# Optimization experiments

Hardware: AMD Instinct MI355X
Metric: run time of the kernel (lower is better)

## Reference

```python
import jax, jax.numpy as jnp
import numpy as np
from jax import lax

TAGSET_SIZE = 50
K = TAGSET_SIZE + 2          # +START, +STOP
START_TAG = TAGSET_SIZE      # 50
STOP_TAG = TAGSET_SIZE + 1   # 51
B, T = 1024, 512
NEG_INF = -10000.0


def setup_inputs() -> dict:
    key = jax.random.key(0)
    k1, k2, k3, k4 = jax.random.split(key, 4)
    logits = jax.random.normal(k1, (B, T, K), dtype=jnp.float32)
    transitions = jax.random.normal(k2, (K, K), dtype=jnp.float32)
    labels = jax.random.randint(k3, (B, T), 0, TAGSET_SIZE)          # real tags only
    lens = jax.random.randint(k4, (B,), 1, T + 1)                    # at least 1 token
    return {"logits": logits, "transitions": transitions, "labels": labels, "lens": lens}


def _crf_nll(logits, transitions, labels, lens):
    b, t, k = logits.shape

    # ---- forward algorithm (log partition) ----
    alpha0 = jnp.full((b, k), NEG_INF, dtype=logits.dtype).at[:, START_TAG].set(0.0)
    step_mask = jnp.arange(t)[None, :] < lens[:, None]               # [B,T] True while c_lens > 0

    def step(alpha, inp):
        logit_t, m_t = inp                                           # [B,K], [B]
        # alpha_nxt[b,i] = logsumexp_j(trans[i,j] + alpha[b,j]) + logit[b,i]
        mat = alpha[:, None, :] + transitions[None, :, :]            # [B,K,K]
        alpha_nxt = jax.nn.logsumexp(mat, axis=2) + logit_t
        alpha = jnp.where(m_t[:, None], alpha_nxt, alpha)
        return alpha, None

    alpha, _ = lax.scan(step, alpha0, (jnp.swapaxes(logits, 0, 1), step_mask.T))
    alpha = alpha + transitions[STOP_TAG][None, :]
    partition = jax.nn.logsumexp(alpha, axis=1)                      # [B]

    # ---- transition score of gold path ----
    start_col = jnp.full((b, 1), START_TAG, dtype=labels.dtype)
    stop_col = jnp.full((b, 1), STOP_TAG, dtype=labels.dtype)
    labels_ext = jnp.concatenate([start_col, labels, stop_col], axis=1)  # [B,T+2]
    pos = jnp.arange(t + 2)[None, :]
    keep = pos < (lens + 1)[:, None]                                 # positions <= lens keep tag, rest -> STOP
    labels_ext = jnp.where(keep, labels_ext, STOP_TAG)
    prev, nxt = labels_ext[:, :-1], labels_ext[:, 1:]                # [B,T+1]
    trn_scr = transitions[nxt, prev]                                 # trans[next, prev]
    m_trn = (jnp.arange(t + 1)[None, :] < (lens + 1)[:, None]).astype(logits.dtype)
    transition_score = jnp.sum(trn_scr * m_trn, axis=1)              # [B]

    # ---- emission score of gold path ----
    em = jnp.take_along_axis(logits, labels[:, :, None], axis=2)[:, :, 0]  # [B,T]
    m_em = (jnp.arange(t)[None, :] < lens[:, None]).astype(logits.dtype)
    emission_score = jnp.sum(em * m_em, axis=1)                      # [B]

    # faithful to source: partition + emission - transition
    return partition + emission_score - transition_score


def reference(logits, transitions, labels, lens):
    return _crf_nll(logits, transitions, labels, lens)
```

## Files before the change

kernel.cpp:

```cpp
#include <hip/hip_runtime.h>
#include <hip/hip_bf16.h>

#define KTAG 52
#define START_TAG 50
#define STOP_TAG 51
#define TMAX 512

__device__ __forceinline__ float rdlane(float v, int l) {
    return __int_as_float(__builtin_amdgcn_readlane(__float_as_int(v), l));
}

__global__ __launch_bounds__(64) void crf_nll_kernel(
    const float* __restrict__ logits,
    const float* __restrict__ trans,
    const int*   __restrict__ labels,
    const int*   __restrict__ lens,
    float* __restrict__ out)
{
    constexpr float L2E = 1.4426950408889634f;
    constexpr float LN2 = 0.6931471805599453f;

    const int b    = blockIdx.x;
    const int lane = threadIdx.x;
    const bool active = lane < KTAG;
    const int len = lens[b];

    float Erow[KTAG];
    {
        const float* trow = trans + (size_t)(active ? lane : 0) * KTAG;
        #pragma unroll
        for (int j = 0; j < KTAG; ++j)
            Erow[j] = active ? exp2f(trow[j] * L2E) : 0.0f;
    }

    const float* lgp = logits + (size_t)b * TMAX * KTAG + (active ? lane : 0);

    float beta = (lane == START_TAG) ? 1.0f : 0.0f;
    float M2 = 0.0f;

    auto lgt = [&](int t) -> float {
        int tc = t < TMAX ? t : (TMAX - 1);
        return lgp[tc * KTAG];
    };

    auto STEP = [&](float lg, float scl) {
        float e = exp2f(lg * L2E) * scl;
        float a0 = 0.f, a1 = 0.f, a2 = 0.f, a3 = 0.f;
        #pragma unroll
        for (int j = 0; j < 13; ++j) {
            a0 = fmaf(Erow[4*j+0], rdlane(beta, 4*j+0), a0);
            a1 = fmaf(Erow[4*j+1], rdlane(beta, 4*j+1), a1);
            a2 = fmaf(Erow[4*j+2], rdlane(beta, 4*j+2), a2);
            a3 = fmaf(Erow[4*j+3], rdlane(beta, 4*j+3), a3);
        }
        beta = ((a0 + a1) + (a2 + a3)) * e;
    };

    float l0 = lgt(0), l1 = lgt(1), l2 = lgt(2), l3 = lgt(3);

    int t = 0;
    while (t + 4 <= len) {
        float n0 = lgt(t + 4), n1 = lgt(t + 5), n2 = lgt(t + 6), n3 = lgt(t + 7);
        float scl = 1.0f;
        if (t > 0) {
            float m = rdlane(beta, 0);
            M2 += log2f(m);
            scl = 1.0f / m;
        }
        STEP(l0, scl);
        STEP(l1, 1.0f);
        STEP(l2, 1.0f);
        STEP(l3, 1.0f);
        l0 = n0; l1 = n1; l2 = n2; l3 = n3;
        t += 4;
    }
    if (t < len) {
        float scl = 1.0f;
        if (t > 0) {
            float m = rdlane(beta, 0);
            M2 += log2f(m);
            scl = 1.0f / m;
        }
        STEP(l0, scl); ++t;
        if (t < len) { STEP(l1, 1.0f); ++t; }
        if (t < len) { STEP(l2, 1.0f); ++t; }
    }

    float es = active ? trans[(size_t)STOP_TAG * KTAG + lane] : 0.0f;
    float contrib = active ? beta * exp2f(es * L2E) : 0.0f;
    float s = contrib;
    #pragma unroll
    for (int off = 32; off; off >>= 1) s += __shfl_xor(s, off);
    float partition = LN2 * (M2 + log2f(s));

    const int*   labp = labels + (size_t)b * TMAX;
    const float* lgb  = logits + (size_t)b * TMAX * KTAG;
    float em = 0.0f, tr = 0.0f;
    for (int tt = lane; tt < len; tt += 64) {
        int lab = labp[tt];
        em += lgb[tt * KTAG + lab];
        int prv = (tt == 0) ? START_TAG : labp[tt - 1];
        tr += trans[lab * KTAG + prv];
    }
    if (lane == 0)
        tr += trans[STOP_TAG * KTAG + labp[len - 1]];

    #pragma unroll
    for (int off = 32; off; off >>= 1) {
        em += __shfl_xor(em, off);
        tr += __shfl_xor(tr, off);
    }

    if (lane == 0) out[b] = partition + em - tr;
}

extern "C" void kernel_launch(void* const* d_in, const int* in_sizes, int n_in,
                              void* d_out, int out_size, void* d_ws, size_t ws_size,
                              hipStream_t stream) {
    const float* logits = (const float*)d_in[0];
    const float* trans  = (const float*)d_in[1];
    const int*   labels = (const int*)d_in[2];
    const int*   lens   = (const int*)d_in[3];
    float* out = (float*)d_out;

    const int B = in_sizes[3];
    crf_nll_kernel<<<dim3(B), dim3(64), 0, stream>>>(logits, trans, labels, lens, out);
}
```

Before: 116.7 us.

## Sort sequences by length and pair short with long per wavefront

Adds a rank kernel that builds a length-sorted permutation of the batch. Each wavefront then processes two sequences, the i-th shortest and the i-th longest, interleaving the two recurrences to balance work and hide latency. The matrix-vector step now reads beta from shared memory with packed FMA instead of 52 readlane broadcasts. This costs an extra kernel launch and workspace use, and adds an LDS write/read dependency on every step.

```diff
diff --git a/kernel.cpp b/kernel.cpp
--- a/kernel.cpp
+++ b/kernel.cpp
@@ -6,112 +6,169 @@
 #define STOP_TAG 51
 #define TMAX 512
 
+typedef float v2f __attribute__((ext_vector_type(2)));
+
 __device__ __forceinline__ float rdlane(float v, int l) {
     return __int_as_float(__builtin_amdgcn_readlane(__float_as_int(v), l));
 }
 
-__global__ __launch_bounds__(64) void crf_nll_kernel(
+__device__ __forceinline__ void pk_fma(v2f& acc, v2f a, v2f b) {
+    asm("v_pk_fma_f32 %0, %1, %2, %0" : "+v"(acc) : "v"(a), "v"(b));
+}
+
+#define LPL 16
+__global__ __launch_bounds__(64) void rank_kernel(
+    const int* __restrict__ lens, int* __restrict__ perm, int B)
+{
+    const int lane = threadIdx.x;
+    int myl[LPL];
+    #pragma unroll
+    for (int k = 0; k < LPL; ++k) {
+        int j = lane * LPL + k;
+        myl[k] = (j < B) ? lens[j] : 0x7fffffff;
+    }
+    const int base = blockIdx.x * 64;
+    for (int i = 0; i < 64; ++i) {
+        int b = base + i;
+        if (b >= B) break;
+        int Lb = lens[b];
+        int r = 0;
+        #pragma unroll
+        for (int k = 0; k < LPL; ++k) {
+            int j = lane * LPL + k;
+            r += (myl[k] < Lb || (myl[k] == Lb && j < b)) ? 1 : 0;
+        }
+        #pragma unroll
+        for (int off = 32; off; off >>= 1) r += __shfl_xor(r, off);
+        if (lane == 0) perm[r] = b;
+    }
+}
+
+__global__ __launch_bounds__(64) void crf_pair_kernel(
     const float* __restrict__ logits,
     const float* __restrict__ trans,
     const int*   __restrict__ labels,
     const int*   __restrict__ lens,
-    float* __restrict__ out)
+    const int*   __restrict__ perm,
+    float* __restrict__ out, int B)
 {
     constexpr float L2E = 1.4426950408889634f;
     constexpr float LN2 = 0.6931471805599453f;
 
-    const int b    = blockIdx.x;
+    const int w    = blockIdx.x;
     const int lane = threadIdx.x;
     const bool active = lane < KTAG;
-    const int len = lens[b];
 
-    float Erow[KTAG];
+    const int iA = w, iB = B - 1 - w;
+    const bool hasB = (iB != iA);
+    const int bA = perm[iA];
+    const int bB = hasB ? perm[iB] : bA;
+    const int nA = lens[bA];
+    const int nB = lens[bB];
+
+    __shared__ __align__(16) float sA[64], sB[64];
+
+    v2f Epk[26];
+    float stopE;
     {
         const float* trow = trans + (size_t)(active ? lane : 0) * KTAG;
         #pragma unroll
-        for (int j = 0; j < KTAG; ++j)
-            Erow[j] = active ? exp2f(trow[j] * L2E) : 0.0f;
+        for (int p = 0; p < 13; ++p) {
+            float4 q = *reinterpret_cast<const float4*>(&trow[4 * p]);
+            v2f lo, hi;
+            lo.x = active ? exp2f(q.x * L2E) : 0.f;
+            lo.y = active ? exp2f(q.y * L2E) : 0.f;
+            hi.x = active ? exp2f(q.z * L2E) : 0.f;
+            hi.y = active ? exp2f(q.w * L2E) : 0.f;
+            Epk[2 * p] = lo; Epk[2 * p + 1] = hi;
+        }
+        stopE = active ? exp2f(trans[(size_t)STOP_TAG * KTAG + lane] * L2E) : 0.f;
     }
 
-    const float* lgp = logits + (size_t)b * TMAX * KTAG + (active ? lane : 0);
+    const float* lgA = logits + (size_t)bA * TMAX * KTAG + (active ? lane : 0);
+    const float* lgB = logits + (size_t)bB * TMAX * KTAG + (active ? lane : 0);
 
-    float beta = (lane == START_TAG) ? 1.0f : 0.0f;
-    float M2 = 0.0f;
+    float betaA = (lane == START_TAG) ? 1.f : 0.f;
+    float betaB = betaA;
+    sA[lane] = betaA;
+    sB[lane] = betaB;
+    float M2A = 0.f, M2B = 0.f;
 
-    auto lgt = [&](int t) -> float {
-        int tc = t < TMAX ? t : (TMAX - 1);
-        return lgp[tc * KTAG];
+    auto ldA = [&](int t) { int tc = t < TMAX ? t : (TMAX - 1); return lgA[tc * KTAG]; };
+    auto ldB = [&](int t) { int tc = t < TMAX ? t : (TMAX - 1); return lgB[tc * KTAG]; };
+
+    float a0 = ldA(0), a1 = ldA(1), a2 = ldA(2), a3 = ldA(3);
+    float b0 = ldB(0), b1 = ldB(1), b2 = ldB(2), b3 = ldB(3);
+
+    auto MATV = [&](float* s, float e) -> float {
+        v2f ac0 = {0.f, 0.f}, ac1 = {0.f, 0.f};
+        #pragma unroll
+        for (int p = 0; p < 13; ++p) {
+            float4 q = *reinterpret_cast<const float4*>(&s[4 * p]);
+            v2f lo; lo.x = q.x; lo.y = q.y;
+            v2f hi; hi.x = q.z; hi.y = q.w;
+            pk_fma(ac0, Epk[2 * p], lo);
+            pk_fma(ac1, Epk[2 * p + 1], hi);
+        }
+        return ((ac0.x + ac0.y) + (ac1.x + ac1.y)) * e;
     };
 
-    auto STEP = [&](float lg, float scl) {
-        float e = exp2f(lg * L2E) * scl;
-        float a0 = 0.f, a1 = 0.f, a2 = 0.f, a3 = 0.f;
+    int t = 0;
+    for (; t < nA; ++t) {
+        float sclA = 1.f, sclB = 1.f;
+        if (((t & 3) == 0) && t) {
+            float mA = rdlane(betaA, 0), mB = rdlane(betaB, 0);
+            M2A += log2f(mA); M2B += log2f(mB);
+            sclA = 1.f / mA;  sclB = 1.f / mB;
+        }
+        float eA = exp2f(a0 * L2E) * sclA;
+        a0 = a1; a1 = a2; a2 = a3; a3 = ldA(t + 4);
+        betaA = MATV(sA, eA);
+        sA[lane] = betaA;
+        float eB = exp2f(b0 * L2E) * sclB;
+        b0 = b1; b1 = b2; b2 = b3; b3 = ldB(t + 4);
+        betaB = MATV(sB, eB);
+        sB[lane] = betaB;
+    }
+    for (; t < nB; ++t) {
+        float sclB = 1.f;
+        if (((t & 3) == 0) && t) {
+            float mB = rdlane(betaB, 0);
+            M2B += log2f(mB);
+            sclB = 1.f / mB;
+        }
+        float eB = exp2f(b0 * L2E) * sclB;
+        b0 = b1; b1 = b2; b2 = b3; b3 = ldB(t + 4);
+        betaB = MATV(sB, eB);
+        sB[lane] = betaB;
+    }
+
+    auto FINISH = [&](float beta, float M2, int b, int len) {
+        float s = beta * stopE;
         #pragma unroll
-        for (int j = 0; j < 13; ++j) {
-            a0 = fmaf(Erow[4*j+0], rdlane(beta, 4*j+0), a0);
-            a1 = fmaf(Erow[4*j+1], rdlane(beta, 4*j+1), a1);
-            a2 = fmaf(Erow[4*j+2], rdlane(beta, 4*j+2), a2);
-            a3 = fmaf(Erow[4*j+3], rdlane(beta, 4*j+3), a3);
+        for (int off = 32; off; off >>= 1) s += __shfl_xor(s, off);
+        float partition = LN2 * (M2 + log2f(s));
+
+        const int*   labp = labels + (size_t)b * TMAX;
+        const float* lgb  = logits + (size_t)b * TMAX * KTAG;
+        float em = 0.f, tr = 0.f;
+        for (int tt = lane; tt < len; tt += 64) {
+            int lab = labp[tt];
+            em += lgb[tt * KTAG + lab];
+            int prv = (tt == 0) ? START_TAG : labp[tt - 1];
+            tr += trans[lab * KTAG + prv];
         }
-        beta = ((a0 + a1) + (a2 + a3)) * e;
+        if (lane == 0) tr += trans[STOP_TAG * KTAG + labp[len - 1]];
+        #pragma unroll
+        for (int off = 32; off; off >>= 1) {
+            em += __shfl_xor(em, off);
+            tr += __shfl_xor(tr, off);
+        }
+        if (lane == 0) out[b] = partition + em - tr;
     };
 
-    float l0 = lgt(0), l1 = lgt(1), l2 = lgt(2), l3 = lgt(3);
-
-    int t = 0;
-    while (t + 4 <= len) {
-        float n0 = lgt(t + 4), n1 = lgt(t + 5), n2 = lgt(t + 6), n3 = lgt(t + 7);
-        float scl = 1.0f;
-        if (t > 0) {
-            float m = rdlane(beta, 0);
-            M2 += log2f(m);
-            scl = 1.0f / m;
-        }
-        STEP(l0, scl);
-        STEP(l1, 1.0f);
-        STEP(l2, 1.0f);
-        STEP(l3, 1.0f);
-        l0 = n0; l1 = n1; l2 = n2; l3 = n3;
-        t += 4;
-    }
-    if (t < len) {
-        float scl = 1.0f;
-        if (t > 0) {
-            float m = rdlane(beta, 0);
-            M2 += log2f(m);
-            scl = 1.0f / m;
-        }
-        STEP(l0, scl); ++t;
-        if (t < len) { STEP(l1, 1.0f); ++t; }
-        if (t < len) { STEP(l2, 1.0f); ++t; }
-    }
-
-    float es = active ? trans[(size_t)STOP_TAG * KTAG + lane] : 0.0f;
-    float contrib = active ? beta * exp2f(es * L2E) : 0.0f;
-    float s = contrib;
-    #pragma unroll
-    for (int off = 32; off; off >>= 1) s += __shfl_xor(s, off);
-    float partition = LN2 * (M2 + log2f(s));
-
-    const int*   labp = labels + (size_t)b * TMAX;
-    const float* lgb  = logits + (size_t)b * TMAX * KTAG;
-    float em = 0.0f, tr = 0.0f;
-    for (int tt = lane; tt < len; tt += 64) {
-        int lab = labp[tt];
-        em += lgb[tt * KTAG + lab];
-        int prv = (tt == 0) ? START_TAG : labp[tt - 1];
-        tr += trans[lab * KTAG + prv];
-    }
-    if (lane == 0)
-        tr += trans[STOP_TAG * KTAG + labp[len - 1]];
-
-    #pragma unroll
-    for (int off = 32; off; off >>= 1) {
-        em += __shfl_xor(em, off);
-        tr += __shfl_xor(tr, off);
-    }
-
-    if (lane == 0) out[b] = partition + em - tr;
+    FINISH(betaA, M2A, bA, nA);
+    if (hasB) FINISH(betaB, M2B, bB, nB);
 }
 
 extern "C" void kernel_launch(void* const* d_in, const int* in_sizes, int n_in,
@@ -124,5 +181,9 @@
     float* out = (float*)d_out;
 
     const int B = in_sizes[3];
-    crf_nll_kernel<<<dim3(B), dim3(64), 0, stream>>>(logits, trans, labels, lens, out);
+    int* perm = (int*)d_ws;
+
+    rank_kernel<<<dim3((B + 63) / 64), dim3(64), 0, stream>>>(lens, perm, B);
+    crf_pair_kernel<<<dim3((B + 1) / 2), dim3(64), 0, stream>>>(
+        logits, trans, labels, lens, perm, out, B);
 }
```

New measurement: 209.8 us. +79.8%, slower.

## Split CRF forward recursion into forward/backward halves and sort batches by length

Applied to the files above, without the earlier changes.

Each sequence is now processed by two waves: one runs the forward recursion over the first half of the timesteps, the other runs a backward recursion over the second half, and the two are combined with a dot product to form the partition. This halves the serial dependency chain per sequence. A separate rank kernel computes a length-sorted permutation so that blocks are interleaved across CUs for load balance. The cost is an extra kernel launch, a workspace buffer, and a shared-memory sync, and the backward wave also does the gold-path scoring.

```diff
diff --git a/kernel.cpp b/kernel.cpp
--- a/kernel.cpp
+++ b/kernel.cpp
@@ -5,113 +5,174 @@
 #define START_TAG 50
 #define STOP_TAG 51
 #define TMAX 512
+#define NCU 256
 
 __device__ __forceinline__ float rdlane(float v, int l) {
     return __int_as_float(__builtin_amdgcn_readlane(__float_as_int(v), l));
 }
 
-__global__ __launch_bounds__(64) void crf_nll_kernel(
+__device__ __forceinline__ float matv(const float* __restrict__ Erow, float v) {
+    float a0 = 0.f, a1 = 0.f, a2 = 0.f, a3 = 0.f;
+    #pragma unroll
+    for (int j = 0; j < 13; ++j) {
+        a0 = fmaf(Erow[4*j+0], rdlane(v, 4*j+0), a0);
+        a1 = fmaf(Erow[4*j+1], rdlane(v, 4*j+1), a1);
+        a2 = fmaf(Erow[4*j+2], rdlane(v, 4*j+2), a2);
+        a3 = fmaf(Erow[4*j+3], rdlane(v, 4*j+3), a3);
+    }
+    return (a0 + a1) + (a2 + a3);
+}
+
+template<bool BWD>
+__device__ __forceinline__ float chain(const float* __restrict__ p0, int stride,
+                                       int maxk, int nsteps, const float* __restrict__ Erow,
+                                       float beta, float& M2) {
+    constexpr float L2E = 1.4426950408889634f;
+    M2 = 0.f;
+
+    auto lgt = [&](int k) -> float {
+        int kc = k < maxk ? k : maxk;
+        return p0[(long)stride * kc];
+    };
+    auto STEP = [&](float lg, float scl) {
+        float e = exp2f(lg * L2E) * scl;
+        if (BWD) beta = matv(Erow, beta * e);
+        else     beta = matv(Erow, beta) * e;
+    };
+
+    float l0 = lgt(0), l1 = lgt(1), l2 = lgt(2), l3 = lgt(3);
+    int k = 0;
+    while (k + 4 <= nsteps) {
+        float n0 = lgt(k+4), n1 = lgt(k+5), n2 = lgt(k+6), n3 = lgt(k+7);
+        float scl = 1.f;
+        if (k > 0) {
+            float m = rdlane(beta, 0);
+            M2 += log2f(m);
+            scl = 1.f / m;
+        }
+        STEP(l0, scl); STEP(l1, 1.f); STEP(l2, 1.f); STEP(l3, 1.f);
+        l0 = n0; l1 = n1; l2 = n2; l3 = n3;
+        k += 4;
+    }
+    if (k < nsteps) {
+        float scl = 1.f;
+        if (k > 0) {
+            float m = rdlane(beta, 0);
+            M2 += log2f(m);
+            scl = 1.f / m;
+        }
+        STEP(l0, scl); ++k;
+        if (k < nsteps) { STEP(l1, 1.f); ++k; }
+        if (k < nsteps) { STEP(l2, 1.f); ++k; }
+    }
+    return beta;
+}
+
+#define LPL 16
+__global__ __launch_bounds__(64) void rank_kernel(
+    const int* __restrict__ lens, int* __restrict__ perm, int B)
+{
+    const int lane = threadIdx.x;
+    int myl[LPL];
+    #pragma unroll
+    for (int k = 0; k < LPL; ++k) {
+        int j = lane * LPL + k;
+        myl[k] = (j < B) ? lens[j] : 0x7fffffff;
+    }
+    const int base = blockIdx.x * 64;
+    for (int i = 0; i < 64; ++i) {
+        int b = base + i;
+        if (b >= B) break;
+        int Lb = lens[b];
+        int r = 0;
+        #pragma unroll
+        for (int k = 0; k < LPL; ++k) {
+            int j = lane * LPL + k;
+            r += (myl[k] < Lb || (myl[k] == Lb && j < b)) ? 1 : 0;
+        }
+        #pragma unroll
+        for (int off = 32; off; off >>= 1) r += __shfl_xor(r, off);
+        if (lane == 0) perm[r] = b;
+    }
+}
+
+__global__ __launch_bounds__(128) void crf_split_kernel(
     const float* __restrict__ logits,
     const float* __restrict__ trans,
     const int*   __restrict__ labels,
     const int*   __restrict__ lens,
-    float* __restrict__ out)
+    const int*   __restrict__ perm,
+    float* __restrict__ out, int B)
 {
     constexpr float L2E = 1.4426950408889634f;
     constexpr float LN2 = 0.6931471805599453f;
 
-    const int b    = blockIdx.x;
-    const int lane = threadIdx.x;
+    const int blk  = blockIdx.x;
+    const int wave = threadIdx.x >> 6;
+    const int lane = threadIdx.x & 63;
     const bool active = lane < KTAG;
-    const int len = lens[b];
+    const bool bwd = (wave == 1);
+
+    int r = blk;
+    if ((B % NCU) == 0) {
+        int per = B / NCU;
+        r = (blk % NCU) * per + (blk / NCU);
+    }
+    const int batch = perm[r];
+    const int len = lens[batch];
+    const int mid = len >> 1;
 
     float Erow[KTAG];
-    {
-        const float* trow = trans + (size_t)(active ? lane : 0) * KTAG;
-        #pragma unroll
-        for (int j = 0; j < KTAG; ++j)
-            Erow[j] = active ? exp2f(trow[j] * L2E) : 0.0f;
+    #pragma unroll
+    for (int j = 0; j < KTAG; ++j) {
+        float tv = active ? (bwd ? trans[j * KTAG + lane]
+                                 : trans[(size_t)lane * KTAG + j]) : 0.f;
+        Erow[j] = active ? exp2f(tv * L2E) : 0.f;
     }
 
-    const float* lgp = logits + (size_t)b * TMAX * KTAG + (active ? lane : 0);
+    const float* base = logits + (size_t)batch * TMAX * KTAG + (active ? lane : 0);
 
-    float beta = (lane == START_TAG) ? 1.0f : 0.0f;
-    float M2 = 0.0f;
-
-    auto lgt = [&](int t) -> float {
-        int tc = t < TMAX ? t : (TMAX - 1);
-        return lgp[tc * KTAG];
-    };
-
-    auto STEP = [&](float lg, float scl) {
-        float e = exp2f(lg * L2E) * scl;
-        float a0 = 0.f, a1 = 0.f, a2 = 0.f, a3 = 0.f;
-        #pragma unroll
-        for (int j = 0; j < 13; ++j) {
-            a0 = fmaf(Erow[4*j+0], rdlane(beta, 4*j+0), a0);
-            a1 = fmaf(Erow[4*j+1], rdlane(beta, 4*j+1), a1);
-            a2 = fmaf(Erow[4*j+2], rdlane(beta, 4*j+2), a2);
-            a3 = fmaf(Erow[4*j+3], rdlane(beta, 4*j+3), a3);
-        }
-        beta = ((a0 + a1) + (a2 + a3)) * e;
-    };
-
-    float l0 = lgt(0), l1 = lgt(1), l2 = lgt(2), l3 = lgt(3);
-
-    int t = 0;
-    while (t + 4 <= len) {
-        float n0 = lgt(t + 4), n1 = lgt(t + 5), n2 = lgt(t + 6), n3 = lgt(t + 7);
-        float scl = 1.0f;
-        if (t > 0) {
-            float m = rdlane(beta, 0);
-            M2 += log2f(m);
-            scl = 1.0f / m;
-        }
-        STEP(l0, scl);
-        STEP(l1, 1.0f);
-        STEP(l2, 1.0f);
-        STEP(l3, 1.0f);
-        l0 = n0; l1 = n1; l2 = n2; l3 = n3;
-        t += 4;
-    }
-    if (t < len) {
-        float scl = 1.0f;
-        if (t > 0) {
-            float m = rdlane(beta, 0);
-            M2 += log2f(m);
-            scl = 1.0f / m;
-        }
-        STEP(l0, scl); ++t;
-        if (t < len) { STEP(l1, 1.0f); ++t; }
-        if (t < len) { STEP(l2, 1.0f); ++t; }
+    float M2, beta;
+    if (bwd) {
+        float b0 = active ? exp2f(trans[STOP_TAG * KTAG + lane] * L2E) : 0.f;
+        beta = chain<true>(base + (size_t)(len - 1) * KTAG, -KTAG,
+                           len - 1, len - mid, Erow, b0, M2);
+    } else {
+        float b0 = (lane == START_TAG) ? 1.f : 0.f;
+        beta = chain<false>(base, KTAG, TMAX - 1, mid, Erow, b0, M2);
     }
 
-    float es = active ? trans[(size_t)STOP_TAG * KTAG + lane] : 0.0f;
-    float contrib = active ? beta * exp2f(es * L2E) : 0.0f;
-    float s = contrib;
-    #pragma unroll
-    for (int off = 32; off; off >>= 1) s += __shfl_xor(s, off);
-    float partition = LN2 * (M2 + log2f(s));
+    __shared__ float sB[64];
+    __shared__ float sM2f;
+    if (!bwd) {
+        sB[lane] = beta;
+        if (lane == 0) sM2f = M2;
+    }
+    __syncthreads();
 
-    const int*   labp = labels + (size_t)b * TMAX;
-    const float* lgb  = logits + (size_t)b * TMAX * KTAG;
-    float em = 0.0f, tr = 0.0f;
-    for (int tt = lane; tt < len; tt += 64) {
-        int lab = labp[tt];
-        em += lgb[tt * KTAG + lab];
-        int prv = (tt == 0) ? START_TAG : labp[tt - 1];
-        tr += trans[lab * KTAG + prv];
+    if (bwd) {
+        float d = beta * sB[lane];
+        #pragma unroll
+        for (int off = 32; off; off >>= 1) d += __shfl_xor(d, off);
+        float partition = LN2 * (sM2f + M2 + log2f(d));
+
+        const int*   labp = labels + (size_t)batch * TMAX;
+        const float* lgb  = logits + (size_t)batch * TMAX * KTAG;
+        float em = 0.f, tr = 0.f;
+        for (int tt = lane; tt < len; tt += 64) {
+            int lab = labp[tt];
+            em += lgb[tt * KTAG + lab];
+            int prv = (tt == 0) ? START_TAG : labp[tt - 1];
+            tr += trans[lab * KTAG + prv];
+        }
+        if (lane == 0) tr += trans[STOP_TAG * KTAG + labp[len - 1]];
+        #pragma unroll
+        for (int off = 32; off; off >>= 1) {
+            em += __shfl_xor(em, off);
+            tr += __shfl_xor(tr, off);
+        }
+        if (lane == 0) out[batch] = partition + em - tr;
     }
-    if (lane == 0)
-        tr += trans[STOP_TAG * KTAG + labp[len - 1]];
-
-    #pragma unroll
-    for (int off = 32; off; off >>= 1) {
-        em += __shfl_xor(em, off);
-        tr += __shfl_xor(tr, off);
-    }
-
-    if (lane == 0) out[b] = partition + em - tr;
 }
 
 extern "C" void kernel_launch(void* const* d_in, const int* in_sizes, int n_in,
@@ -124,5 +185,9 @@
     float* out = (float*)d_out;
 
     const int B = in_sizes[3];
-    crf_nll_kernel<<<dim3(B), dim3(64), 0, stream>>>(logits, trans, labels, lens, out);
+    int* perm = (int*)d_ws;
+
+    rank_kernel<<<dim3((B + 63) / 64), dim3(64), 0, stream>>>(lens, perm, B);
+    crf_split_kernel<<<dim3(B), dim3(128), 0, stream>>>(
+        logits, trans, labels, lens, perm, out, B);
 }
```

Measured after the change: 152.2 us. 30.5% more time.

## Run forward and backward CRF recursions concurrently meeting at sequence midpoint

Applied to the files above, without the earlier changes.

Splits the serial forward-algorithm recursion into a forward pass over the first half and a backward pass over the second half, interleaved in the same wavefront. The partition is recovered by a dot product of the two messages at the midpoint. This roughly halves the length of the serial dependency chain per batch row, at the cost of twice the registers for transition matrices (forward and transposed copies) and more readlane traffic per step. The gold-path score loop is also unrolled with all loads issued before the reduction.

```diff
diff --git a/kernel.cpp b/kernel.cpp
--- a/kernel.cpp
+++ b/kernel.cpp
@@ -1,16 +1,15 @@
 #include <hip/hip_runtime.h>
-#include <hip/hip_bf16.h>
 
 #define KTAG 52
 #define START_TAG 50
 #define STOP_TAG 51
 #define TMAX 512
 
-__device__ __forceinline__ float rdlane(float v, int l) {
+__device__ __forceinline__ float rdlanef(float v, int l) {
     return __int_as_float(__builtin_amdgcn_readlane(__float_as_int(v), l));
 }
 
-__global__ __launch_bounds__(64) void crf_nll_kernel(
+__global__ __launch_bounds__(64, 1) void crf_fused_kernel(
     const float* __restrict__ logits,
     const float* __restrict__ trans,
     const int*   __restrict__ labels,
@@ -24,87 +23,133 @@
     const int lane = threadIdx.x;
     const bool active = lane < KTAG;
     const int len = lens[b];
+    const int mid = len >> 1;
 
-    float Erow[KTAG];
-    {
-        const float* trow = trans + (size_t)(active ? lane : 0) * KTAG;
-        #pragma unroll
-        for (int j = 0; j < KTAG; ++j)
-            Erow[j] = active ? exp2f(trow[j] * L2E) : 0.0f;
+    float EF[KTAG], EB[KTAG];
+    #pragma unroll
+    for (int j = 0; j < KTAG; ++j) {
+        float tf = active ? trans[(size_t)lane * KTAG + j] : 0.f;
+        float tb = active ? trans[(size_t)j * KTAG + lane] : 0.f;
+        EF[j] = active ? exp2f(tf * L2E) : 0.f;
+        EB[j] = active ? exp2f(tb * L2E) : 0.f;
     }
 
-    const float* lgp = logits + (size_t)b * TMAX * KTAG + (active ? lane : 0);
+    const float* pF = logits + (size_t)b * TMAX * KTAG + (active ? lane : 0);
+    const float* pB = pF + (size_t)(len - 1) * KTAG;
 
-    float beta = (lane == START_TAG) ? 1.0f : 0.0f;
-    float M2 = 0.0f;
-
-    auto lgt = [&](int t) -> float {
-        int tc = t < TMAX ? t : (TMAX - 1);
-        return lgp[tc * KTAG];
+    auto lgF = [&](int k) -> float {
+        int kc = k < TMAX - 1 ? k : TMAX - 1;
+        return pF[(long)KTAG * kc];
+    };
+    auto lgB = [&](int k) -> float {
+        int kc = k < len - 1 ? k : len - 1;
+        return pB[-(long)KTAG * kc];
     };
 
-    auto STEP = [&](float lg, float scl) {
-        float e = exp2f(lg * L2E) * scl;
+    float betaF = (lane == START_TAG) ? 1.f : 0.f;
+    float gamma = active ? exp2f(trans[STOP_TAG * KTAG + lane] * L2E) : 0.f;
+    float M2F = 0.f, M2B = 0.f;
+
+    auto STEP2 = [&](float lf, float sf, float lb, float sb) {
+        float eF = exp2f(lf * L2E);
+        float eB = exp2f(lb * L2E);
+        float xF = betaF * sf;
+        float xB = gamma * sb * eB;
+        float fa0 = 0.f, fa1 = 0.f, fa2 = 0.f, fa3 = 0.f;
+        float ba0 = 0.f, ba1 = 0.f, ba2 = 0.f, ba3 = 0.f;
+        #pragma unroll
+        for (int p = 0; p < 13; ++p) {
+            fa0 = fmaf(EF[4*p+0], rdlanef(xF, 4*p+0), fa0);
+            ba0 = fmaf(EB[4*p+0], rdlanef(xB, 4*p+0), ba0);
+            fa1 = fmaf(EF[4*p+1], rdlanef(xF, 4*p+1), fa1);
+            ba1 = fmaf(EB[4*p+1], rdlanef(xB, 4*p+1), ba1);
+            fa2 = fmaf(EF[4*p+2], rdlanef(xF, 4*p+2), fa2);
+            ba2 = fmaf(EB[4*p+2], rdlanef(xB, 4*p+2), ba2);
+            fa3 = fmaf(EF[4*p+3], rdlanef(xF, 4*p+3), fa3);
+            ba3 = fmaf(EB[4*p+3], rdlanef(xB, 4*p+3), ba3);
+        }
+        betaF = ((fa0 + fa1) + (fa2 + fa3)) * eF;
+        gamma = ((ba0 + ba1) + (ba2 + ba3));
+    };
+    auto STEPB = [&](float lb, float sb) {
+        float eB = exp2f(lb * L2E);
+        float xB = gamma * sb * eB;
         float a0 = 0.f, a1 = 0.f, a2 = 0.f, a3 = 0.f;
         #pragma unroll
-        for (int j = 0; j < 13; ++j) {
-            a0 = fmaf(Erow[4*j+0], rdlane(beta, 4*j+0), a0);
-            a1 = fmaf(Erow[4*j+1], rdlane(beta, 4*j+1), a1);
-            a2 = fmaf(Erow[4*j+2], rdlane(beta, 4*j+2), a2);
-            a3 = fmaf(Erow[4*j+3], rdlane(beta, 4*j+3), a3);
+        for (int p = 0; p < 13; ++p) {
+            a0 = fmaf(EB[4*p+0], rdlanef(xB, 4*p+0), a0);
+            a1 = fmaf(EB[4*p+1], rdlanef(xB, 4*p+1), a1);
+            a2 = fmaf(EB[4*p+2], rdlanef(xB, 4*p+2), a2);
+            a3 = fmaf(EB[4*p+3], rdlanef(xB, 4*p+3), a3);
         }
-        beta = ((a0 + a1) + (a2 + a3)) * e;
+        gamma = (a0 + a1) + (a2 + a3);
     };
 
-    float l0 = lgt(0), l1 = lgt(1), l2 = lgt(2), l3 = lgt(3);
+    float f0 = lgF(0), f1 = lgF(1), f2 = lgF(2), f3 = lgF(3);
+    float g0 = lgB(0), g1 = lgB(1), g2 = lgB(2), g3 = lgB(3);
 
     int t = 0;
-    while (t + 4 <= len) {
-        float n0 = lgt(t + 4), n1 = lgt(t + 5), n2 = lgt(t + 6), n3 = lgt(t + 7);
-        float scl = 1.0f;
+    while (t + 4 <= mid) {
+        float nf0 = lgF(t+4), nf1 = lgF(t+5), nf2 = lgF(t+6), nf3 = lgF(t+7);
+        float ng0 = lgB(t+4), ng1 = lgB(t+5), ng2 = lgB(t+6), ng3 = lgB(t+7);
+        float sF = 1.f, sB = 1.f;
         if (t > 0) {
-            float m = rdlane(beta, 0);
-            M2 += log2f(m);
-            scl = 1.0f / m;
+            float mF = fmaxf(rdlanef(betaF, 0), 1e-30f);
+            float mB = fmaxf(rdlanef(gamma, 0), 1e-30f);
+            M2F += log2f(mF); sF = 1.f / mF;
+            M2B += log2f(mB); sB = 1.f / mB;
         }
-        STEP(l0, scl);
-        STEP(l1, 1.0f);
-        STEP(l2, 1.0f);
-        STEP(l3, 1.0f);
-        l0 = n0; l1 = n1; l2 = n2; l3 = n3;
+        STEP2(f0, sF, g0, sB);
+        STEP2(f1, 1.f, g1, 1.f);
+        STEP2(f2, 1.f, g2, 1.f);
+        STEP2(f3, 1.f, g3, 1.f);
+        f0 = nf0; f1 = nf1; f2 = nf2; f3 = nf3;
+        g0 = ng0; g1 = ng1; g2 = ng2; g3 = ng3;
         t += 4;
     }
-    if (t < len) {
-        float scl = 1.0f;
+    const int r = mid - t;
+    if (r > 0) {
+        float sF = 1.f, sB = 1.f;
         if (t > 0) {
-            float m = rdlane(beta, 0);
-            M2 += log2f(m);
-            scl = 1.0f / m;
+            float mF = fmaxf(rdlanef(betaF, 0), 1e-30f);
+            float mB = fmaxf(rdlanef(gamma, 0), 1e-30f);
+            M2F += log2f(mF); sF = 1.f / mF;
+            M2B += log2f(mB); sB = 1.f / mB;
         }
-        STEP(l0, scl); ++t;
-        if (t < len) { STEP(l1, 1.0f); ++t; }
-        if (t < len) { STEP(l2, 1.0f); ++t; }
+        STEP2(f0, sF, g0, sB);
+        if (r > 1) STEP2(f1, 1.f, g1, 1.f);
+        if (r > 2) STEP2(f2, 1.f, g2, 1.f);
+    }
+    if (len - mid > mid) {
+        float gl = (r == 0) ? g0 : (r == 1) ? g1 : (r == 2) ? g2 : g3;
+        STEPB(gl, 1.f);
     }
 
-    float es = active ? trans[(size_t)STOP_TAG * KTAG + lane] : 0.0f;
-    float contrib = active ? beta * exp2f(es * L2E) : 0.0f;
-    float s = contrib;
+    float d = gamma * betaF;
     #pragma unroll
-    for (int off = 32; off; off >>= 1) s += __shfl_xor(s, off);
-    float partition = LN2 * (M2 + log2f(s));
+    for (int off = 32; off; off >>= 1) d += __shfl_xor(d, off);
+    float partition = LN2 * (M2F + M2B + log2f(d));
 
     const int*   labp = labels + (size_t)b * TMAX;
     const float* lgb  = logits + (size_t)b * TMAX * KTAG;
-    float em = 0.0f, tr = 0.0f;
-    for (int tt = lane; tt < len; tt += 64) {
-        int lab = labp[tt];
-        em += lgb[tt * KTAG + lab];
-        int prv = (tt == 0) ? START_TAG : labp[tt - 1];
-        tr += trans[lab * KTAG + prv];
+    int lab[8], prv[8]; bool msk[8];
+    #pragma unroll
+    for (int c = 0; c < 8; ++c) {
+        int tt = c * 64 + lane;
+        msk[c] = tt < len;
+        int ttc = msk[c] ? tt : 0;
+        lab[c] = labp[ttc];
+        prv[c] = (ttc == 0) ? START_TAG : labp[ttc - 1];
     }
-    if (lane == 0)
-        tr += trans[STOP_TAG * KTAG + labp[len - 1]];
-
+    float em = 0.f, tr = 0.f;
+    #pragma unroll
+    for (int c = 0; c < 8; ++c) {
+        int ttc = msk[c] ? (c * 64 + lane) : 0;
+        float ev = lgb[(size_t)ttc * KTAG + lab[c]];
+        float tv = trans[lab[c] * KTAG + prv[c]];
+        if (msk[c]) { em += ev; tr += tv; }
+    }
+    if (lane == 0) tr += trans[STOP_TAG * KTAG + labp[len - 1]];
     #pragma unroll
     for (int off = 32; off; off >>= 1) {
         em += __shfl_xor(em, off);
@@ -124,5 +169,5 @@
     float* out = (float*)d_out;
 
     const int B = in_sizes[3];
-    crf_nll_kernel<<<dim3(B), dim3(64), 0, stream>>>(logits, trans, labels, lens, out);
+    crf_fused_kernel<<<dim3(B), dim3(64), 0, stream>>>(logits, trans, labels, lens, out);
 }
```

After: 119.3 us. 1.02x slower.
